# Kernel optimization log

Hardware: AMD Instinct MI355X
Metric: run time of the kernel (lower is better)

The kernel has to match this reference:

```python
import jax, jax.numpy as jnp
import numpy as np
import itertools

N_BOX = 19
B = 2048
T = 5
_EDGES = np.array(list(itertools.combinations(range(N_BOX), 2)))  # [E,2], E=171
ROW = jnp.asarray(_EDGES[:, 0])
COL = jnp.asarray(_EDGES[:, 1])


def setup_inputs() -> dict:
    key = jax.random.key(0)
    ks = jax.random.split(key, 8)
    return {
        "location_t": jax.random.uniform(ks[0], (B, N_BOX, 5), dtype=jnp.float32),
        "feature_t": jax.random.normal(ks[1], (B, N_BOX, 512), dtype=jnp.float32),
        "mask_t": jax.random.randint(ks[2], (B, N_BOX), 0, 2).astype(bool),
        "past_location_t": jax.random.uniform(ks[3], (B, T, N_BOX, 6), dtype=jnp.float32),
        "W1": jax.random.normal(ks[4], (512, 256), dtype=jnp.float32) * 0.05,
        "b1": jax.random.normal(ks[5], (256,), dtype=jnp.float32) * 0.05,
        "W2": jax.random.normal(ks[6], (256, 512), dtype=jnp.float32) * 0.05,
        "b2": jax.random.normal(ks[7], (512,), dtype=jnp.float32) * 0.05,
    }


def _edge_weights(location_t, mask, past_location_t):
    # bbox centers from cols 1..4: [B,N]
    cx = 0.5 * (location_t[:, :, 1] + location_t[:, :, 3])
    cy = 0.5 * (location_t[:, :, 2] + location_t[:, :, 4])
    d = (cx[:, ROW] - cx[:, COL]) ** 2 + (cy[:, ROW] - cy[:, COL]) ** 2  # [B,E]

    # motion distance, vectorized over all nodes then gathered per edge
    cp = past_location_t[:, :, :, 3:-1] - past_location_t[:, :, :, 1:3]  # [B,T,N,2]
    cpx = cp[..., 0] * 1280.0  # [B,T,N]
    cpy = cp[..., 1] * 720.0
    dx = cpx[:, -1] - cpx[:, 0]  # [B,N]
    dy = cpy[:, -1] - cpy[:, 0]
    length = jnp.sqrt(dx ** 2 + dy ** 2)
    length = jnp.where(length == 0.0, 1.0, length)
    ndx = dx / length
    ndy = dy / length
    x0 = cpx[:, 0]  # [B,N]
    y0 = cpy[:, 0]
    d1 = jnp.sqrt((x0[:, ROW] + ndx[:, ROW] - x0[:, COL] - ndx[:, COL]) ** 2
                  + (y0[:, ROW] + ndy[:, ROW] - y0[:, COL] - ndy[:, COL]) ** 2)
    d2 = jnp.sqrt((x0[:, ROW] - x0[:, COL]) ** 2 + (y0[:, ROW] - y0[:, COL]) ** 2)
    md = d1 - d2  # [B,E]

    w = jnp.exp(-(0.7 * d + 0.3 * md))
    valid = mask[:, ROW] & mask[:, COL]
    w = jnp.where(valid, w, 0.0)
    wmin = jnp.min(w, axis=1, keepdims=True)
    wmax = jnp.max(w, axis=1, keepdims=True)
    return (w - wmin) / (wmax - wmin)


def _gcn(x, ew, W, b):
    # PyG GCNConv: add self loops (weight 1), symmetric normalization, x@W, scatter-add, +bias
    n = x.shape[0]
    loops = jnp.arange(n)
    row = jnp.concatenate([ROW, loops])
    col = jnp.concatenate([COL, loops])
    ew_full = jnp.concatenate([ew, jnp.ones((n,), ew.dtype)])
    deg = jax.ops.segment_sum(ew_full, col, num_segments=n)
    dinv = jnp.where(deg > 0, deg ** -0.5, 0.0)
    norm = dinv[row] * ew_full * dinv[col]  # [E+N]
    xw = x @ W  # [N,F_out]
    out = jnp.zeros((n, W.shape[1]), xw.dtype).at[col].add(norm[:, None] * xw[row])
    return out + b


def reference(location_t, feature_t, mask_t, past_location_t, W1, b1, W2, b2):
    w = _edge_weights(location_t, mask_t, past_location_t)  # [B,E]

    def per_graph(x, ew):
        h = jax.nn.sigmoid(_gcn(x, ew, W1, b1))
        return jax.nn.sigmoid(_gcn(h, ew, W2, b2))

    return jax.vmap(per_graph)(feature_t, w)  # [B,19,512]
```

## Files before the change

kernel.cpp:

```cpp
#include <hip/hip_runtime.h>
#include <hip/hip_bf16.h>
#include <math.h>

#define NBOX 19
#define NEDGE 171
#define TT 5
#define BATCH 2048
#define MROWS (BATCH * NBOX)

typedef __attribute__((ext_vector_type(8))) short short8v;
typedef __attribute__((ext_vector_type(4))) float f32x4;

static __device__ __forceinline__ ushort f2bf(float f) {
    __hip_bfloat16 h = __float2bfloat16(f);
    return *reinterpret_cast<ushort*>(&h);
}

__device__ __forceinline__ int edge_index(int r, int c) {
    return r * (NBOX - 1) - (r * (r - 1)) / 2 + (c - r - 1);
}

__global__ __launch_bounds__(192) void adj_kernel(
    const float* __restrict__ loc,
    const int*   __restrict__ mask,
    const float* __restrict__ past,
    float* __restrict__ adj)
{
    int b = blockIdx.x;
    int tid = threadIdx.x;
    __shared__ float cx[NBOX], cy[NBOX], x0[NBOX], y0[NBOX], ndx[NBOX], ndy[NBOX];
    __shared__ int   mv[NBOX];
    __shared__ float w[NEDGE];
    __shared__ float dinv[NBOX];
    __shared__ float wmin_s, wmax_s;

    if (tid < NBOX) {
        const float* l = loc + ((size_t)b * NBOX + tid) * 5;
        cx[tid] = 0.5f * (l[1] + l[3]);
        cy[tid] = 0.5f * (l[2] + l[4]);
        const float* p0 = past + (((size_t)b * TT + 0) * NBOX + tid) * 6;
        const float* p4 = past + (((size_t)b * TT + (TT - 1)) * NBOX + tid) * 6;
        float cpx0 = (p0[3] - p0[1]) * 1280.0f, cpy0 = (p0[4] - p0[2]) * 720.0f;
        float cpx4 = (p4[3] - p4[1]) * 1280.0f, cpy4 = (p4[4] - p4[2]) * 720.0f;
        float dx = cpx4 - cpx0, dy = cpy4 - cpy0;
        float len = sqrtf(dx * dx + dy * dy);
        if (len == 0.0f) len = 1.0f;
        ndx[tid] = dx / len;
        ndy[tid] = dy / len;
        x0[tid] = cpx0;
        y0[tid] = cpy0;
        mv[tid] = mask[(size_t)b * NBOX + tid];
    }
    __syncthreads();

    float wv = 0.0f;
    if (tid < NEDGE) {
        int rem = tid, rr = 0;
        while (rem >= NBOX - 1 - rr) { rem -= NBOX - 1 - rr; rr++; }
        int r = rr, c = rr + 1 + rem;
        float ddx = cx[r] - cx[c], ddy = cy[r] - cy[c];
        float d = ddx * ddx + ddy * ddy;
        float ax = x0[r] + ndx[r] - x0[c] - ndx[c];
        float ay = y0[r] + ndy[r] - y0[c] - ndy[c];
        float d1 = sqrtf(ax * ax + ay * ay);
        float bx = x0[r] - x0[c], by = y0[r] - y0[c];
        float d2 = sqrtf(bx * bx + by * by);
        float md = d1 - d2;
        wv = expf(-(0.7f * d + 0.3f * md));
        if (!(mv[r] && mv[c])) wv = 0.0f;
        w[tid] = wv;
    }
    __syncthreads();

    if (tid == 0) {
        float mn = w[0], mx = w[0];
        for (int i = 1; i < NEDGE; i++) { mn = fminf(mn, w[i]); mx = fmaxf(mx, w[i]); }
        wmin_s = mn; wmax_s = mx;
    }
    __syncthreads();

    float inv_range = 1.0f / (wmax_s - wmin_s);
    if (tid < NEDGE) w[tid] = (wv - wmin_s) * inv_range;
    __syncthreads();

    if (tid < NBOX) {
        float s = 1.0f;
        for (int rr = 0; rr < tid; rr++) s += w[edge_index(rr, tid)];
        dinv[tid] = 1.0f / sqrtf(s);
    }
    __syncthreads();

    float* A = adj + (size_t)b * NBOX * NBOX;
    for (int idx = tid; idx < NBOX * NBOX; idx += blockDim.x) {
        int rr = idx % NBOX, cc = idx / NBOX;
        float v = 0.0f;
        if (rr == cc) v = dinv[rr] * dinv[rr];
        else if (rr < cc) v = w[edge_index(rr, cc)] * dinv[rr] * dinv[cc];
        A[idx] = v;
    }
}

__global__ void packT_kernel(const float* __restrict__ src, ushort* __restrict__ dst,
                             int K, int N)
{
    int total = K * N;
    for (int idx = blockIdx.x * blockDim.x + threadIdx.x; idx < total;
         idx += gridDim.x * blockDim.x) {
        int n = idx / K, k = idx % K;
        dst[idx] = f2bf(src[(size_t)k * N + n]);
    }
}

template<int AF32>
__global__ __launch_bounds__(256) void gemm_bf16_kernel(
    const void* __restrict__ Ag_, const ushort* __restrict__ BT,
    float* __restrict__ Y, int K, int N)
{
    constexpr int BM = 128, BN = 64, BK = 64;
    __shared__ __align__(16) ushort As[BM * BK];
    __shared__ __align__(16) ushort Bs[BN * BK];

    const int tid = threadIdx.x;
    const int lane = tid & 63, wid = tid >> 6;
    const int wm = wid >> 1, wn = wid & 1;
    const int bM = blockIdx.x, bN = blockIdx.y;

    f32x4 acc[4][2];
#pragma unroll
    for (int fm = 0; fm < 4; fm++)
#pragma unroll
        for (int fn = 0; fn < 2; fn++)
            acc[fm][fn] = (f32x4){0.0f, 0.0f, 0.0f, 0.0f};

    for (int k0 = 0; k0 < K; k0 += BK) {
        __syncthreads();
        if constexpr (AF32) {
            const float* Ag = (const float*)Ag_;
            int r = tid >> 4, g = tid & 15;
#pragma unroll
            for (int p = 0; p < 8; p++) {
                int row = r + p * 16;
                const float4 v = *(const float4*)(Ag + ((size_t)(bM * BM + row)) * K + k0 + g * 4);
                ushort4 h;
                h.x = f2bf(v.x); h.y = f2bf(v.y); h.z = f2bf(v.z); h.w = f2bf(v.w);
                int boff = (row * 128 + g * 8) ^ ((row & 7) << 4);
                *(ushort4*)((char*)As + boff) = h;
            }
        } else {
            const ushort* Ag = (const ushort*)Ag_;
            int r = tid >> 3, g = tid & 7;
#pragma unroll
            for (int p = 0; p < 4; p++) {
                int row = r + p * 32;
                const int4 v = *(const int4*)(Ag + ((size_t)(bM * BM + row)) * K + k0 + g * 8);
                int boff = (row * 128 + g * 16) ^ ((row & 7) << 4);
                *(int4*)((char*)As + boff) = v;
            }
        }
        {
            int r = tid >> 3, g = tid & 7;
#pragma unroll
            for (int p = 0; p < 2; p++) {
                int n = r + p * 32;
                const int4 v = *(const int4*)(BT + ((size_t)(bN * BN + n)) * K + k0 + g * 8);
                int boff = (n * 128 + g * 16) ^ ((n & 7) << 4);
                *(int4*)((char*)Bs + boff) = v;
            }
        }
        __syncthreads();

#pragma unroll
        for (int ks = 0; ks < 2; ks++) {
            short8v a[4], bb[2];
#pragma unroll
            for (int fm = 0; fm < 4; fm++) {
                int row = wm * 64 + fm * 16 + (lane & 15);
                int boff = (row * 128 + ks * 64 + (lane >> 4) * 16) ^ ((row & 7) << 4);
                a[fm] = *(short8v*)((char*)As + boff);
            }
#pragma unroll
            for (int fn = 0; fn < 2; fn++) {
                int n = wn * 32 + fn * 16 + (lane & 15);
                int boff = (n * 128 + ks * 64 + (lane >> 4) * 16) ^ ((n & 7) << 4);
                bb[fn] = *(short8v*)((char*)Bs + boff);
            }
#pragma unroll
            for (int fm = 0; fm < 4; fm++)
#pragma unroll
                for (int fn = 0; fn < 2; fn++)
                    acc[fm][fn] = __builtin_amdgcn_mfma_f32_16x16x32_bf16(
                        a[fm], bb[fn], acc[fm][fn], 0, 0, 0);
        }
    }

#pragma unroll
    for (int fm = 0; fm < 4; fm++) {
        int grow0 = bM * BM + wm * 64 + fm * 16 + (lane >> 4) * 4;
#pragma unroll
        for (int fn = 0; fn < 2; fn++) {
            int gcol = bN * BN + wn * 32 + fn * 16 + (lane & 15);
#pragma unroll
            for (int j = 0; j < 4; j++) {
                Y[(size_t)(grow0 + j) * N + gcol] = acc[fm][fn][j];
            }
        }
    }
}

__global__ __launch_bounds__(256) void agg1_kernel(
    const float* __restrict__ Y1, const float* __restrict__ adj,
    const float* __restrict__ b1, ushort* __restrict__ H)
{
    int b = blockIdx.x, j = threadIdx.x;
    __shared__ float As[NBOX * NBOX];
    for (int i = j; i < NBOX * NBOX; i += 256) As[i] = adj[(size_t)b * NBOX * NBOX + i];
    __syncthreads();

    const float* Yb = Y1 + (size_t)b * NBOX * 256;
    float y[NBOX];
#pragma unroll
    for (int r = 0; r < NBOX; r++) y[r] = Yb[r * 256 + j];
    float bj = b1[j];
    ushort* Hb = H + (size_t)b * NBOX * 256;
#pragma unroll
    for (int cc = 0; cc < NBOX; cc++) {
        float s = bj;
#pragma unroll
        for (int r = 0; r < NBOX; r++) s = fmaf(As[cc * NBOX + r], y[r], s);
        Hb[cc * 256 + j] = f2bf(1.0f / (1.0f + expf(-s)));
    }
}

__global__ __launch_bounds__(256) void agg2_kernel(
    const float* __restrict__ adj, const float* __restrict__ b2, float* Y)
{
    int b = blockIdx.x, j = threadIdx.x;
    __shared__ float As[NBOX * NBOX];
    for (int i = j; i < NBOX * NBOX; i += 256) As[i] = adj[(size_t)b * NBOX * NBOX + i];
    __syncthreads();

    float* Yb = Y + (size_t)b * NBOX * 512;
    float y0[NBOX], y1[NBOX];
#pragma unroll
    for (int r = 0; r < NBOX; r++) {
        y0[r] = Yb[r * 512 + j];
        y1[r] = Yb[r * 512 + j + 256];
    }
    float bj0 = b2[j], bj1 = b2[j + 256];
#pragma unroll
    for (int cc = 0; cc < NBOX; cc++) {
        float s0 = bj0, s1 = bj1;
#pragma unroll
        for (int r = 0; r < NBOX; r++) {
            float a = As[cc * NBOX + r];
            s0 = fmaf(a, y0[r], s0);
            s1 = fmaf(a, y1[r], s1);
        }
        Yb[cc * 512 + j]       = 1.0f / (1.0f + expf(-s0));
        Yb[cc * 512 + j + 256] = 1.0f / (1.0f + expf(-s1));
    }
}

extern "C" void kernel_launch(void* const* d_in, const int* in_sizes, int n_in,
                              void* d_out, int out_size, void* d_ws, size_t ws_size,
                              hipStream_t stream) {
    const float* loc  = (const float*)d_in[0];
    const float* feat = (const float*)d_in[1];
    const int*   mask = (const int*)d_in[2];
    const float* past = (const float*)d_in[3];
    const float* W1   = (const float*)d_in[4];
    const float* b1   = (const float*)d_in[5];
    const float* W2   = (const float*)d_in[6];
    const float* b2   = (const float*)d_in[7];

    float*  adj = (float*)d_ws;
    ushort* W1T = (ushort*)(adj + (size_t)BATCH * NBOX * NBOX);
    ushort* W2T = W1T + 256 * 512;
    ushort* H   = W2T + 512 * 256;

    float* Y1 = (float*)d_out;
    float* Y2 = (float*)d_out;

    adj_kernel<<<BATCH, 192, 0, stream>>>(loc, mask, past, adj);
    packT_kernel<<<512, 256, 0, stream>>>(W1, W1T, 512, 256);
    packT_kernel<<<512, 256, 0, stream>>>(W2, W2T, 256, 512);

    gemm_bf16_kernel<1><<<dim3(MROWS / 128, 256 / 64), 256, 0, stream>>>(
        feat, W1T, Y1, 512, 256);
    agg1_kernel<<<BATCH, 256, 0, stream>>>(Y1, adj, b1, H);
    gemm_bf16_kernel<0><<<dim3(MROWS / 128, 512 / 64), 256, 0, stream>>>(
        H, W2T, Y2, 256, 512);
    agg2_kernel<<<BATCH, 256, 0, stream>>>(adj, b2, Y2);
}
```

Measured before the change: 128.6 us.

## Fuse both GCN layers into one kernel with MFMA-based graph aggregation

```diff
diff --git a/kernel.cpp b/kernel.cpp
--- a/kernel.cpp
+++ b/kernel.cpp
@@ -6,7 +6,9 @@
 #define NEDGE 171
 #define TT 5
 #define BATCH 2048
-#define MROWS (BATCH * NBOX)
+#define GB 4
+#define MR (GB * NBOX)
+#define MP 80
 
 typedef __attribute__((ext_vector_type(8))) short short8v;
 typedef __attribute__((ext_vector_type(4))) float f32x4;
@@ -20,11 +22,11 @@
     return r * (NBOX - 1) - (r * (r - 1)) / 2 + (c - r - 1);
 }
 
-__global__ __launch_bounds__(192) void adj_kernel(
+__global__ __launch_bounds__(192) void adjbf_kernel(
     const float* __restrict__ loc,
     const int*   __restrict__ mask,
     const float* __restrict__ past,
-    float* __restrict__ adj)
+    ushort* __restrict__ adjbf)
 {
     int b = blockIdx.x;
     int tid = threadIdx.x;
@@ -90,13 +92,15 @@
     }
     __syncthreads();
 
-    float* A = adj + (size_t)b * NBOX * NBOX;
-    for (int idx = tid; idx < NBOX * NBOX; idx += blockDim.x) {
-        int rr = idx % NBOX, cc = idx / NBOX;
+    ushort* A = adjbf + (size_t)b * 1024;
+    for (int idx = tid; idx < 1024; idx += 192) {
+        int r = idx & 31, cc = idx >> 5;
         float v = 0.0f;
-        if (rr == cc) v = dinv[rr] * dinv[rr];
-        else if (rr < cc) v = w[edge_index(rr, cc)] * dinv[rr] * dinv[cc];
-        A[idx] = v;
+        if (r < NBOX && cc < NBOX) {
+            if (r == cc) v = dinv[r] * dinv[r];
+            else if (r < cc) v = w[edge_index(r, cc)] * dinv[r] * dinv[cc];
+        }
+        A[idx] = f2bf(v);
     }
 }
 
@@ -111,153 +115,197 @@
     }
 }
 
-template<int AF32>
-__global__ __launch_bounds__(256) void gemm_bf16_kernel(
-    const void* __restrict__ Ag_, const ushort* __restrict__ BT,
-    float* __restrict__ Y, int K, int N)
+__global__ __launch_bounds__(256) void fused_kernel(
+    const float*  __restrict__ feat,
+    const ushort* __restrict__ adjbf,
+    const ushort* __restrict__ W1T,
+    const ushort* __restrict__ W2T,
+    const float*  __restrict__ b1,
+    const float*  __restrict__ b2,
+    float* __restrict__ out)
 {
-    constexpr int BM = 128, BN = 64, BK = 64;
-    __shared__ __align__(16) ushort As[BM * BK];
-    __shared__ __align__(16) ushort Bs[BN * BK];
+    __shared__ __align__(16) ushort Xs[MP * 256];
+    __shared__ __align__(16) ushort Hs[MP * 256];
+    __shared__ __align__(16) ushort YsT[64 * 128];
+    __shared__ __align__(16) ushort AdjS[GB * 32 * 40];
 
     const int tid = threadIdx.x;
-    const int lane = tid & 63, wid = tid >> 6;
-    const int wm = wid >> 1, wn = wid & 1;
-    const int bM = blockIdx.x, bN = blockIdx.y;
-
-    f32x4 acc[4][2];
-#pragma unroll
-    for (int fm = 0; fm < 4; fm++)
-#pragma unroll
-        for (int fn = 0; fn < 2; fn++)
-            acc[fm][fn] = (f32x4){0.0f, 0.0f, 0.0f, 0.0f};
-
-    for (int k0 = 0; k0 < K; k0 += BK) {
-        __syncthreads();
-        if constexpr (AF32) {
-            const float* Ag = (const float*)Ag_;
-            int r = tid >> 4, g = tid & 15;
-#pragma unroll
-            for (int p = 0; p < 8; p++) {
-                int row = r + p * 16;
-                const float4 v = *(const float4*)(Ag + ((size_t)(bM * BM + row)) * K + k0 + g * 4);
-                ushort4 h;
-                h.x = f2bf(v.x); h.y = f2bf(v.y); h.z = f2bf(v.z); h.w = f2bf(v.w);
-                int boff = (row * 128 + g * 8) ^ ((row & 7) << 4);
-                *(ushort4*)((char*)As + boff) = h;
-            }
-        } else {
-            const ushort* Ag = (const ushort*)Ag_;
-            int r = tid >> 3, g = tid & 7;
-#pragma unroll
-            for (int p = 0; p < 4; p++) {
-                int row = r + p * 32;
-                const int4 v = *(const int4*)(Ag + ((size_t)(bM * BM + row)) * K + k0 + g * 8);
-                int boff = (row * 128 + g * 16) ^ ((row & 7) << 4);
-                *(int4*)((char*)As + boff) = v;
-            }
-        }
-        {
-            int r = tid >> 3, g = tid & 7;
-#pragma unroll
-            for (int p = 0; p < 2; p++) {
-                int n = r + p * 32;
-                const int4 v = *(const int4*)(BT + ((size_t)(bN * BN + n)) * K + k0 + g * 8);
-                int boff = (n * 128 + g * 16) ^ ((n & 7) << 4);
-                *(int4*)((char*)Bs + boff) = v;
-            }
-        }
-        __syncthreads();
-
-#pragma unroll
-        for (int ks = 0; ks < 2; ks++) {
-            short8v a[4], bb[2];
-#pragma unroll
-            for (int fm = 0; fm < 4; fm++) {
-                int row = wm * 64 + fm * 16 + (lane & 15);
-                int boff = (row * 128 + ks * 64 + (lane >> 4) * 16) ^ ((row & 7) << 4);
-                a[fm] = *(short8v*)((char*)As + boff);
-            }
-#pragma unroll
-            for (int fn = 0; fn < 2; fn++) {
-                int n = wn * 32 + fn * 16 + (lane & 15);
-                int boff = (n * 128 + ks * 64 + (lane >> 4) * 16) ^ ((n & 7) << 4);
-                bb[fn] = *(short8v*)((char*)Bs + boff);
-            }
-#pragma unroll
-            for (int fm = 0; fm < 4; fm++)
-#pragma unroll
-                for (int fn = 0; fn < 2; fn++)
-                    acc[fm][fn] = __builtin_amdgcn_mfma_f32_16x16x32_bf16(
-                        a[fm], bb[fn], acc[fm][fn], 0, 0, 0);
-        }
-    }
-
-#pragma unroll
-    for (int fm = 0; fm < 4; fm++) {
-        int grow0 = bM * BM + wm * 64 + fm * 16 + (lane >> 4) * 4;
-#pragma unroll
-        for (int fn = 0; fn < 2; fn++) {
-            int gcol = bN * BN + wn * 32 + fn * 16 + (lane & 15);
+    const int lane = tid & 63, w = tid >> 6;
+    const int rowbase = blockIdx.x * MR;
+    const int bbase = blockIdx.x * GB;
+    const int ncol = w * 16 + (lane & 15);
+    const int kgrp = (lane >> 4);
+
+    {
+        const int4* src = (const int4*)(adjbf + (size_t)bbase * 1024);
+#pragma unroll
+        for (int p = 0; p < 2; p++) {
+            int ii = tid + p * 256;
+            int g = ii >> 7, rem = ii & 127;
+            int cc = rem >> 2, kk = rem & 3;
+            *(int4*)((char*)AdjS + g * 2560 + cc * 80 + kk * 16) = src[ii];
+        }
+    }
+#pragma unroll
+    for (int p = 0; p < 4; p++)
+        ((int4*)YsT)[tid + p * 256] = make_int4(0, 0, 0, 0);
+
+    f32x4 acc1[4][5];
+#pragma unroll
+    for (int c = 0; c < 4; c++)
+#pragma unroll
+        for (int m = 0; m < 5; m++) acc1[c][m] = (f32x4){0.f, 0.f, 0.f, 0.f};
+
+    for (int kh = 0; kh < 2; kh++) {
+        __syncthreads();
+        const float* fg = feat + (size_t)rowbase * 512 + kh * 256;
+#pragma unroll 4
+        for (int p = 0; p < 19; p++) {
+            int i = tid + p * 256;
+            int row = i >> 6, q = i & 63;
+            float4 v = *(const float4*)(fg + (size_t)row * 512 + q * 4);
+            ushort4 h;
+            h.x = f2bf(v.x); h.y = f2bf(v.y); h.z = f2bf(v.z); h.w = f2bf(v.w);
+            int boff = (row * 512 + q * 8) ^ ((row & 7) << 4);
+            *(ushort4*)((char*)Xs + boff) = h;
+        }
+        __syncthreads();
+
+#pragma unroll
+        for (int c = 0; c < 4; c++) {
+            const ushort* bp = W1T + (size_t)(c * 64 + ncol) * 512 + kh * 256 + kgrp * 8;
+            short8v bring[2];
+            bring[0] = *(const short8v*)(bp);
+            bring[1] = *(const short8v*)(bp + 32);
+#pragma unroll
+            for (int ks = 0; ks < 8; ks++) {
+                short8v bcur = bring[ks & 1];
+                if (ks + 2 < 8) bring[ks & 1] = *(const short8v*)(bp + (ks + 2) * 32);
+                short8v a[5];
+#pragma unroll
+                for (int m = 0; m < 5; m++) {
+                    int row = m * 16 + (lane & 15);
+                    int boff = (row * 512 + ks * 64 + kgrp * 16) ^ ((row & 7) << 4);
+                    a[m] = *(const short8v*)((char*)Xs + boff);
+                }
+#pragma unroll
+                for (int m = 0; m < 5; m++)
+                    acc1[c][m] = __builtin_amdgcn_mfma_f32_16x16x32_bf16(
+                        a[m], bcur, acc1[c][m], 0, 0, 0);
+            }
+        }
+    }
+
+#pragma unroll 1
+    for (int c = 0; c < 4; c++) {
+        __syncthreads();
+#pragma unroll
+        for (int m = 0; m < 5; m++) {
 #pragma unroll
             for (int j = 0; j < 4; j++) {
-                Y[(size_t)(grow0 + j) * N + gcol] = acc[fm][fn][j];
-            }
-        }
-    }
-}
-
-__global__ __launch_bounds__(256) void agg1_kernel(
-    const float* __restrict__ Y1, const float* __restrict__ adj,
-    const float* __restrict__ b1, ushort* __restrict__ H)
-{
-    int b = blockIdx.x, j = threadIdx.x;
-    __shared__ float As[NBOX * NBOX];
-    for (int i = j; i < NBOX * NBOX; i += 256) As[i] = adj[(size_t)b * NBOX * NBOX + i];
-    __syncthreads();
-
-    const float* Yb = Y1 + (size_t)b * NBOX * 256;
-    float y[NBOX];
-#pragma unroll
-    for (int r = 0; r < NBOX; r++) y[r] = Yb[r * 256 + j];
-    float bj = b1[j];
-    ushort* Hb = H + (size_t)b * NBOX * 256;
-#pragma unroll
-    for (int cc = 0; cc < NBOX; cc++) {
-        float s = bj;
-#pragma unroll
-        for (int r = 0; r < NBOX; r++) s = fmaf(As[cc * NBOX + r], y[r], s);
-        Hb[cc * 256 + j] = f2bf(1.0f / (1.0f + expf(-s)));
-    }
-}
-
-__global__ __launch_bounds__(256) void agg2_kernel(
-    const float* __restrict__ adj, const float* __restrict__ b2, float* Y)
-{
-    int b = blockIdx.x, j = threadIdx.x;
-    __shared__ float As[NBOX * NBOX];
-    for (int i = j; i < NBOX * NBOX; i += 256) As[i] = adj[(size_t)b * NBOX * NBOX + i];
-    __syncthreads();
-
-    float* Yb = Y + (size_t)b * NBOX * 512;
-    float y0[NBOX], y1[NBOX];
-#pragma unroll
-    for (int r = 0; r < NBOX; r++) {
-        y0[r] = Yb[r * 512 + j];
-        y1[r] = Yb[r * 512 + j + 256];
-    }
-    float bj0 = b2[j], bj1 = b2[j + 256];
-#pragma unroll
-    for (int cc = 0; cc < NBOX; cc++) {
-        float s0 = bj0, s1 = bj1;
-#pragma unroll
-        for (int r = 0; r < NBOX; r++) {
-            float a = As[cc * NBOX + r];
-            s0 = fmaf(a, y0[r], s0);
-            s1 = fmaf(a, y1[r], s1);
-        }
-        Yb[cc * 512 + j]       = 1.0f / (1.0f + expf(-s0));
-        Yb[cc * 512 + j + 256] = 1.0f / (1.0f + expf(-s1));
+                int gr = m * 16 + kgrp * 4 + j;
+                if (gr < MR) {
+                    int g = gr / 19, r = gr - g * 19;
+                    int boff = (ncol * 256 + (g * 32 + r) * 2) ^ ((ncol & 7) << 4);
+                    *(ushort*)((char*)YsT + boff) = f2bf(acc1[c][m][j]);
+                }
+            }
+        }
+        __syncthreads();
+        float bv = b1[c * 64 + ncol];
+        short8v yb[GB];
+#pragma unroll
+        for (int g = 0; g < GB; g++) {
+            int boff = (ncol * 256 + g * 64 + kgrp * 16) ^ ((ncol & 7) << 4);
+            yb[g] = *(const short8v*)((char*)YsT + boff);
+        }
+#pragma unroll
+        for (int g = 0; g < GB; g++) {
+#pragma unroll
+            for (int mt = 0; mt < 2; mt++) {
+                short8v af = *(const short8v*)((char*)AdjS + g * 2560 +
+                                               (mt * 16 + (lane & 15)) * 80 + kgrp * 16);
+                f32x4 o = __builtin_amdgcn_mfma_f32_16x16x32_bf16(
+                    af, yb[g], (f32x4){0.f, 0.f, 0.f, 0.f}, 0, 0, 0);
+#pragma unroll
+                for (int j = 0; j < 4; j++) {
+                    int cc = mt * 16 + kgrp * 4 + j;
+                    if (cc < NBOX) {
+                        float s = 1.0f / (1.0f + expf(-(o[j] + bv)));
+                        int gr = g * 19 + cc;
+                        int boff = (gr * 512 + (c * 64 + ncol) * 2) ^ ((gr & 7) << 4);
+                        *(ushort*)((char*)Hs + boff) = f2bf(s);
+                    }
+                }
+            }
+        }
+    }
+    __syncthreads();
+
+#pragma unroll 1
+    for (int c = 0; c < 8; c++) {
+        f32x4 acc[5];
+#pragma unroll
+        for (int m = 0; m < 5; m++) acc[m] = (f32x4){0.f, 0.f, 0.f, 0.f};
+        const int n0 = c * 64 + ncol;
+        const ushort* bp = W2T + (size_t)n0 * 256 + kgrp * 8;
+        short8v bring[2];
+        bring[0] = *(const short8v*)(bp);
+        bring[1] = *(const short8v*)(bp + 32);
+#pragma unroll
+        for (int ks = 0; ks < 8; ks++) {
+            short8v bcur = bring[ks & 1];
+            if (ks + 2 < 8) bring[ks & 1] = *(const short8v*)(bp + (ks + 2) * 32);
+            short8v a[5];
+#pragma unroll
+            for (int m = 0; m < 5; m++) {
+                int row = m * 16 + (lane & 15);
+                int boff = (row * 512 + ks * 64 + kgrp * 16) ^ ((row & 7) << 4);
+                a[m] = *(const short8v*)((char*)Hs + boff);
+            }
+#pragma unroll
+            for (int m = 0; m < 5; m++)
+                acc[m] = __builtin_amdgcn_mfma_f32_16x16x32_bf16(a[m], bcur, acc[m], 0, 0, 0);
+        }
+        __syncthreads();
+#pragma unroll
+        for (int m = 0; m < 5; m++) {
+#pragma unroll
+            for (int j = 0; j < 4; j++) {
+                int gr = m * 16 + kgrp * 4 + j;
+                if (gr < MR) {
+                    int g = gr / 19, r = gr - g * 19;
+                    int boff = (ncol * 256 + (g * 32 + r) * 2) ^ ((ncol & 7) << 4);
+                    *(ushort*)((char*)YsT + boff) = f2bf(acc[m][j]);
+                }
+            }
+        }
+        __syncthreads();
+        float bv = b2[n0];
+        short8v yb[GB];
+#pragma unroll
+        for (int g = 0; g < GB; g++) {
+            int boff = (ncol * 256 + g * 64 + kgrp * 16) ^ ((ncol & 7) << 4);
+            yb[g] = *(const short8v*)((char*)YsT + boff);
+        }
+#pragma unroll
+        for (int g = 0; g < GB; g++) {
+#pragma unroll
+            for (int mt = 0; mt < 2; mt++) {
+                short8v af = *(const short8v*)((char*)AdjS + g * 2560 +
+                                               (mt * 16 + (lane & 15)) * 80 + kgrp * 16);
+                f32x4 o = __builtin_amdgcn_mfma_f32_16x16x32_bf16(
+                    af, yb[g], (f32x4){0.f, 0.f, 0.f, 0.f}, 0, 0, 0);
+#pragma unroll
+                for (int j = 0; j < 4; j++) {
+                    int cc = mt * 16 + kgrp * 4 + j;
+                    if (cc < NBOX) {
+                        float s = 1.0f / (1.0f + expf(-(o[j] + bv)));
+                        out[((size_t)(bbase + g) * NBOX + cc) * 512 + n0] = s;
+                    }
+                }
+            }
+        }
     }
 }
 
@@ -273,22 +321,14 @@
     const float* W2   = (const float*)d_in[6];
     const float* b2   = (const float*)d_in[7];
 
-    float*  adj = (float*)d_ws;
-    ushort* W1T = (ushort*)(adj + (size_t)BATCH * NBOX * NBOX);
-    ushort* W2T = W1T + 256 * 512;
-    ushort* H   = W2T + 512 * 256;
-
-    float* Y1 = (float*)d_out;
-    float* Y2 = (float*)d_out;
-
-    adj_kernel<<<BATCH, 192, 0, stream>>>(loc, mask, past, adj);
+    ushort* adjbf = (ushort*)d_ws;
+    ushort* W1T   = adjbf + (size_t)BATCH * 1024;
+    ushort* W2T   = W1T + 256 * 512;
+
+    adjbf_kernel<<<BATCH, 192, 0, stream>>>(loc, mask, past, adjbf);
     packT_kernel<<<512, 256, 0, stream>>>(W1, W1T, 512, 256);
-    packT_kernel<<<512, 256, 0, stream>>>(W2, W2T, 256, 512);
-
-    gemm_bf16_kernel<1><<<dim3(MROWS / 128, 256 / 64), 256, 0, stream>>>(
-        feat, W1T, Y1, 512, 256);
-    agg1_kernel<<<BATCH, 256, 0, stream>>>(Y1, adj, b1, H);
-    gemm_bf16_kernel<0><<<dim3(MROWS / 128, 512 / 64), 256, 0, stream>>>(
-        H, W2T, Y2, 256, 512);
-    agg2_kernel<<<BATCH, 256, 0, stream>>>(adj, b2, Y2);
-}
+    packT_kernel<<<256, 256, 0, stream>>>(W2, W2T, 256, 512);
+
+    fused_kernel<<<BATCH / GB, 256, 0, stream>>>(feat, adjbf, W1T, W2T, b1, b2,
+                                                 (float*)d_out);
+}
```

Result: slower. 163.5 us (+27.2%).
